# Kernel tuning notes

Hardware: AMD Instinct MI355X
Metric: run time of the kernel (lower is better)

Reference implementation:

```python
import jax, jax.numpy as jnp
import numpy as np

N = 200000          # nodes
E = 6400000         # edges (before self-loops)
L = 4               # layer_n
H = 9               # hidden_channels (hardcoded in module)
G = 2000            # graphs in batch
C = 2               # num_classes
NEG_SLOPE = 0.2     # GATConv default leaky_relu slope for attention logits


def setup_inputs() -> dict:
    key = jax.random.key(0)
    ks = jax.random.split(key, 9)
    x = jax.random.normal(ks[0], (N, H), dtype=jnp.float32)
    edge_index = jax.random.randint(ks[1], (2, E), 0, N, dtype=jnp.int32)
    batch = jnp.sort(jax.random.randint(ks[2], (N,), 0, G, dtype=jnp.int32))
    W = jax.random.normal(ks[3], (L, H, H), dtype=jnp.float32) * 0.3
    att_src = jax.random.normal(ks[4], (L, H), dtype=jnp.float32) * 0.3
    att_dst = jax.random.normal(ks[5], (L, H), dtype=jnp.float32) * 0.3
    bias = jax.random.normal(ks[6], (L, H), dtype=jnp.float32) * 0.1
    fc_w = jax.random.normal(ks[7], (L * H, C), dtype=jnp.float32) * 0.2
    fc_b = jax.random.normal(ks[8], (C,), dtype=jnp.float32) * 0.1
    return dict(x=x, edge_index=edge_index, batch=batch, W=W,
                att_src=att_src, att_dst=att_dst, bias=bias,
                fc_w=fc_w, fc_b=fc_b)


def _gat_layer(x, W_l, a_src, a_dst, b_l, src, dst, n):
    # h: [N, H] transformed features (linear, no bias per PyG default)
    h = x @ W_l
    alpha_s = h @ a_src            # [N]
    alpha_d = h @ a_dst            # [N]
    # attention logits per edge (src -> dst), GAT softmax grouped by dst
    e = jax.nn.leaky_relu(alpha_s[src] + alpha_d[dst], NEG_SLOPE)  # [E']
    e = e - jax.ops.segment_max(e, dst, num_segments=n)[dst]
    w = jnp.exp(e)
    denom = jax.ops.segment_sum(w, dst, num_segments=n)[dst]
    alpha = w / denom              # [E']
    out = jax.ops.segment_sum(alpha[:, None] * h[src], dst, num_segments=n)
    return out + b_l


def reference(x, edge_index, batch, W, att_src, att_dst, bias, fc_w, fc_b):
    n = x.shape[0]
    loops = jnp.arange(n, dtype=edge_index.dtype)
    src = jnp.concatenate([edge_index[0], loops])  # add_self_loops=True
    dst = jnp.concatenate([edge_index[1], loops])
    jk = []
    h = x
    for l in range(L):
        h = _gat_layer(h, W[l], att_src[l], att_dst[l], bias[l], src, dst, n)
        h = jax.nn.relu(h)
        jk.append(h)
    jk = jnp.concatenate(jk, axis=1)               # [N, L*H]
    pooled = jax.ops.segment_max(jk, batch, num_segments=G)
    pooled = jnp.where(jnp.isfinite(pooled), pooled, 0.0)  # guard empty graphs
    # dropout is identity at inference
    return pooled @ fc_w + fc_b
```

## Files before the change

### kernel.cpp

```cpp
#include <hip/hip_runtime.h>
#include <hip/hip_fp16.h>

#define Nn 200000
#define Ee 6400000
#define EP 6600000
#define Hh 9
#define Ll 4
#define Gg 2000
#define Cc 2
#define JK 36
#define NCB ((Nn + 1023) >> 10)
#define EPB 8192
#define NBLKA ((EP + EPB - 1) / EPB)
#define NB ((Nn + 255) / 256)
#define NPB 64
#define NAB (Nn / NPB)
#define CAP 4096

union H2F { __half2 h; float f; };


__global__ __launch_bounds__(256) void k_count(
    const int* __restrict__ dst, int* __restrict__ ctot)
{
    __shared__ int lh[NCB];
    int t = threadIdx.x;
    if (t < NCB) lh[t] = 0;
    __syncthreads();
    int base = blockIdx.x * EPB;
    for (int j = 0; j < EPB; j += 256) {
        int e = base + j + t;
        if (e < EP) {
            int d = (e < Ee) ? dst[e] : (e - Ee);
            atomicAdd(&lh[d >> 10], 1);
        }
    }
    __syncthreads();
    if (t < NCB && lh[t]) atomicAdd(&ctot[t], lh[t]);
}

__global__ __launch_bounds__(256) void k_scan(
    const int* __restrict__ ctot, int* __restrict__ cbase,
    int* __restrict__ ccur, int* __restrict__ row_ptr)
{
    __shared__ int s[256];
    int t = threadIdx.x;
    int v = (t < NCB) ? ctot[t] : 0;
    s[t] = v; __syncthreads();
    for (int off = 1; off < 256; off <<= 1) {
        int u = (t >= off) ? s[t - off] : 0;
        __syncthreads();
        s[t] += u;
        __syncthreads();
    }
    if (t < NCB) { cbase[t] = s[t] - v; ccur[t] = s[t] - v; }
    if (t == 0) { cbase[NCB] = EP; row_ptr[Nn] = EP; }
}

__global__ __launch_bounds__(256) void kA_scatter(
    const int* __restrict__ src, const int* __restrict__ dst,
    int* __restrict__ ccur, unsigned* __restrict__ bucketed)
{
    __shared__ int lh[NCB];
    __shared__ int cur[NCB];
    int t = threadIdx.x;
    if (t < NCB) lh[t] = 0;
    __syncthreads();
    int base = blockIdx.x * EPB;
    for (int j = 0; j < EPB; j += 256) {
        int e = base + j + t;
        if (e < EP) {
            int d = (e < Ee) ? dst[e] : (e - Ee);
            atomicAdd(&lh[d >> 10], 1);
        }
    }
    __syncthreads();
    if (t < NCB) cur[t] = atomicAdd(&ccur[t], lh[t]);
    __syncthreads();
    for (int j = 0; j < EPB; j += 256) {
        int e = base + j + t;
        if (e < EP) {
            int s, d;
            if (e < Ee) { s = src[e]; d = dst[e]; } else { s = e - Ee; d = s; }
            int pos = atomicAdd(&cur[d >> 10], 1);
            bucketed[pos] = (unsigned)s | ((unsigned)(d & 1023) << 18);
        }
    }
}

__global__ __launch_bounds__(1024) void kB_csr(
    const unsigned* __restrict__ bucketed, const int* __restrict__ cbase,
    int* __restrict__ row_ptr, int* __restrict__ csr_src)
{
    __shared__ int bh[1024];
    __shared__ int cur[1024];
    int k = blockIdx.x;
    int beg = cbase[k], end = cbase[k + 1];
    int t = threadIdx.x;
    bh[t] = 0;
    __syncthreads();
    for (int i = beg + t; i < end; i += 1024)
        atomicAdd(&bh[(bucketed[i] >> 18) & 1023], 1);
    __syncthreads();
    int v = bh[t];
    for (int off = 1; off < 1024; off <<= 1) {
        int u = (t >= off) ? bh[t - off] : 0;
        __syncthreads();
        bh[t] += u;
        __syncthreads();
    }
    int pos0 = beg + bh[t] - v;
    int node = (k << 10) + t;
    if (node < Nn) row_ptr[node] = pos0;
    cur[t] = pos0;
    __syncthreads();
    for (int i = beg + t; i < end; i += 1024) {
        unsigned p = bucketed[i];
        int pos = atomicAdd(&cur[(p >> 18) & 1023], 1);
        csr_src[pos] = (int)(p & 0x3FFFFu);
    }
}


__global__ __launch_bounds__(256) void k_transform(
    const float* __restrict__ xin, int xstride,
    const float* __restrict__ Wl,
    const float* __restrict__ asrc, const float* __restrict__ adst,
    float* __restrict__ h)
{
    int i = blockIdx.x * blockDim.x + threadIdx.x;
    if (i >= Nn) return;
    const float* xp = xin + (size_t)i * xstride;
    float xi[Hh];
#pragma unroll
    for (int k = 0; k < Hh; ++k) xi[k] = xp[k];
    float hv[Hh];
#pragma unroll
    for (int j = 0; j < Hh; ++j) {
        float s = 0.f;
#pragma unroll
        for (int k = 0; k < Hh; ++k) s += xi[k] * Wl[k * Hh + j];
        hv[j] = s;
    }
    float as = 0.f, ad = 0.f;
#pragma unroll
    for (int j = 0; j < Hh; ++j) { as += hv[j] * asrc[j]; ad += hv[j] * adst[j]; }
    H2F u01, u23, u45, u67, u8p;
    u01.h = __floats2half2_rn(hv[0], hv[1]);
    u23.h = __floats2half2_rn(hv[2], hv[3]);
    u45.h = __floats2half2_rn(hv[4], hv[5]);
    u67.h = __floats2half2_rn(hv[6], hv[7]);
    u8p.h = __floats2half2_rn(hv[8], 0.f);
    float4* hp = (float4*)(h + ((size_t)i << 3));
    hp[0] = make_float4(u01.f, u23.f, u45.f, u67.f);
    hp[1] = make_float4(u8p.f, as, ad, 0.f);
}

__global__ __launch_bounds__(256) void k_node_agg(
    const int* __restrict__ rp, const int* __restrict__ csr,
    const float* __restrict__ h, const float* __restrict__ biasl,
    float* __restrict__ jk, int l)
{
    __shared__ int scsr[CAP];
    __shared__ int srp[NPB + 1];
    const int nbase = blockIdx.x * NPB;
    const int t = threadIdx.x;
    if (t <= NPB) srp[t] = rp[nbase + t];
    __syncthreads();
    const int beg_blk = srp[0];
    const int nseg = srp[NPB] - beg_blk;
    const bool use_lds = (nseg <= CAP);
    if (use_lds)
        for (int j = t; j < nseg; j += 256) scsr[j] = csr[beg_blk + j];
    __syncthreads();

    const int ni = t >> 2;
    const int q  = t & 3;
    const int i  = nbase + ni;
    const float c = h[((size_t)i << 3) + 6];
    float a0=0,a1=0,a2=0,a3=0,a4=0,a5=0,a6=0,a7=0,a8=0,den=0;
    if (use_lds) {
        int idx = srp[ni] - beg_blk + q;
        const int iend = srp[ni + 1] - beg_blk;
        int s = (idx < iend) ? scsr[idx] : 0;
        while (idx < iend) {
            int nidx = idx + 4;
            int sn = (nidx < iend) ? scsr[nidx] : 0;
            const float4* hp = (const float4*)(h + ((size_t)s << 3));
            float4 F0 = hp[0], F1 = hp[1];
            float lg = F1.y + c;
            lg = lg > 0.f ? lg : 0.2f * lg;
            float w = __expf(lg);
            H2F u; float2 p;
            u.f = F0.x; p = __half22float2(u.h); a0 += w*p.x; a1 += w*p.y;
            u.f = F0.y; p = __half22float2(u.h); a2 += w*p.x; a3 += w*p.y;
            u.f = F0.z; p = __half22float2(u.h); a4 += w*p.x; a5 += w*p.y;
            u.f = F0.w; p = __half22float2(u.h); a6 += w*p.x; a7 += w*p.y;
            u.f = F1.x; p = __half22float2(u.h); a8 += w*p.x;
            den += w;
            idx = nidx; s = sn;
        }
    } else {
        for (int e = srp[ni] + q; e < srp[ni + 1]; e += 4) {
            int s = csr[e];
            const float4* hp = (const float4*)(h + ((size_t)s << 3));
            float4 F0 = hp[0], F1 = hp[1];
            float lg = F1.y + c;
            lg = lg > 0.f ? lg : 0.2f * lg;
            float w = __expf(lg);
            H2F u; float2 p;
            u.f = F0.x; p = __half22float2(u.h); a0 += w*p.x; a1 += w*p.y;
            u.f = F0.y; p = __half22float2(u.h); a2 += w*p.x; a3 += w*p.y;
            u.f = F0.z; p = __half22float2(u.h); a4 += w*p.x; a5 += w*p.y;
            u.f = F0.w; p = __half22float2(u.h); a6 += w*p.x; a7 += w*p.y;
            u.f = F1.x; p = __half22float2(u.h); a8 += w*p.x;
            den += w;
        }
    }
#pragma unroll
    for (int m = 1; m <= 2; m <<= 1) {
        a0 += __shfl_xor(a0, m); a1 += __shfl_xor(a1, m);
        a2 += __shfl_xor(a2, m); a3 += __shfl_xor(a3, m);
        a4 += __shfl_xor(a4, m); a5 += __shfl_xor(a5, m);
        a6 += __shfl_xor(a6, m); a7 += __shfl_xor(a7, m);
        a8 += __shfl_xor(a8, m); den += __shfl_xor(den, m);
    }
    if (q == 0) {
        float inv = 1.f / den;
        float* jp = jk + (size_t)i * JK + l * Hh;
        float o;
        o = a0*inv + biasl[0]; jp[0] = fmaxf(o, 0.f);
        o = a1*inv + biasl[1]; jp[1] = fmaxf(o, 0.f);
        o = a2*inv + biasl[2]; jp[2] = fmaxf(o, 0.f);
        o = a3*inv + biasl[3]; jp[3] = fmaxf(o, 0.f);
        o = a4*inv + biasl[4]; jp[4] = fmaxf(o, 0.f);
        o = a5*inv + biasl[5]; jp[5] = fmaxf(o, 0.f);
        o = a6*inv + biasl[6]; jp[6] = fmaxf(o, 0.f);
        o = a7*inv + biasl[7]; jp[7] = fmaxf(o, 0.f);
        o = a8*inv + biasl[8]; jp[8] = fmaxf(o, 0.f);
    }
}


__global__ __launch_bounds__(256) void k_graph_ptr(
    const int* __restrict__ batch, int* __restrict__ gp)
{
    int i = blockIdx.x * 256 + threadIdx.x;
    if (i >= Nn) return;
    int b = batch[i];
    if (i == 0) {
        for (int g = 0; g <= b; ++g) gp[g] = 0;
    } else {
        int pb = batch[i - 1];
        for (int g = pb + 1; g <= b; ++g) gp[g] = i;
    }
    if (i == Nn - 1) {
        for (int g = b + 1; g <= Gg; ++g) gp[g] = Nn;
    }
}

__global__ __launch_bounds__(256) void k_pool_seg(
    const float* __restrict__ jk, const int* __restrict__ gp,
    float* __restrict__ pooled)
{
    int t = blockIdx.x * 256 + threadIdx.x;
    if (t >= Gg * JK) return;
    int g = t / JK, col = t - g * JK;
    int beg = gp[g], end = gp[g + 1];
    float m = 0.f;
    for (int i = beg; i < end; ++i)
        m = fmaxf(m, jk[(size_t)i * JK + col]);
    pooled[t] = m;
}

__global__ __launch_bounds__(256) void k_fc(
    const float* __restrict__ pooled, const float* __restrict__ fcw,
    const float* __restrict__ fcb, float* __restrict__ out)
{
    int t = blockIdx.x * blockDim.x + threadIdx.x;
    if (t >= Gg * Cc) return;
    int g = t / Cc, c = t - g * Cc;
    float s = fcb[c];
    const float* pp = pooled + (size_t)g * JK;
#pragma unroll
    for (int j = 0; j < JK; ++j) s += pp[j] * fcw[j * Cc + c];
    out[t] = s;
}

extern "C" void kernel_launch(void* const* d_in, const int* in_sizes, int n_in,
                              void* d_out, int out_size, void* d_ws, size_t ws_size,
                              hipStream_t stream) {
    const float* x      = (const float*)d_in[0];
    const int*   ei     = (const int*)d_in[1];
    const int*   batch  = (const int*)d_in[2];
    const float* W      = (const float*)d_in[3];
    const float* a_src  = (const float*)d_in[4];
    const float* a_dst  = (const float*)d_in[5];
    const float* bias   = (const float*)d_in[6];
    const float* fc_w   = (const float*)d_in[7];
    const float* fc_b   = (const float*)d_in[8];
    float* out = (float*)d_out;

    float* ws        = (float*)d_ws;
    float* h         = ws;
    float* jk        = h + (size_t)Nn * 8;
    float* pooled    = jk + (size_t)Nn * JK;
    int* row_ptr     = (int*)(pooled + (size_t)Gg * JK);
    int* gp          = row_ptr + Nn + 1;
    int* ctot        = gp + Gg + 1;
    int* cbase       = ctot + NCB;
    int* ccur        = cbase + NCB + 1;
    int* csr_src     = ccur + NCB;
    unsigned* bucketed = (unsigned*)jk;

    const int* srcp = ei;
    const int* dstp = ei + Ee;

    hipMemsetAsync(ctot, 0, NCB * sizeof(int), stream);
    k_count   <<<NBLKA, 256, 0, stream>>>(dstp, ctot);
    k_scan    <<<1, 256, 0, stream>>>(ctot, cbase, ccur, row_ptr);
    kA_scatter<<<NBLKA, 256, 0, stream>>>(srcp, dstp, ccur, bucketed);
    kB_csr    <<<NCB, 1024, 0, stream>>>(bucketed, cbase, row_ptr, csr_src);

    for (int l = 0; l < Ll; ++l) {
        const float* xin = (l == 0) ? x : (jk + (size_t)(l - 1) * Hh);
        int xstride      = (l == 0) ? Hh : JK;
        k_transform<<<NB, 256, 0, stream>>>(xin, xstride, W + l * Hh * Hh,
                                            a_src + l * Hh, a_dst + l * Hh, h);
        k_node_agg<<<NAB, 256, 0, stream>>>(row_ptr, csr_src,
                                            h, bias + l * Hh, jk, l);
    }
    k_graph_ptr<<<NB, 256, 0, stream>>>(batch, gp);
    k_pool_seg<<<(Gg * JK + 255) / 256, 256, 0, stream>>>(jk, gp, pooled);
    k_fc<<<(Gg * Cc + 255) / 256, 256, 0, stream>>>(pooled, fc_w, fc_b, out);
}
```

Measured before the change: 586.5 us.

## Stage bucketed edges in LDS for coalesced writes; use 8 lanes per node

The scatter kernel now sorts each block's edges into an LDS buffer by coarse destination bucket, using a local prefix scan. It then writes them out contiguously per bucket through a binary-search offset lookup, replacing scattered global writes made through shared atomic cursors. The aggregation kernel halves nodes per block and assigns 8 lanes per node instead of 4, with the shuffle reduction widened to match. This trades a larger LDS footprint (32KB buffer) and extra binary-search work for better write coalescing and more parallelism per high-degree node.

```diff
diff --git a/kernel.cpp b/kernel.cpp
--- a/kernel.cpp
+++ b/kernel.cpp
@@ -13,9 +13,9 @@
 #define EPB 8192
 #define NBLKA ((EP + EPB - 1) / EPB)
 #define NB ((Nn + 255) / 256)
-#define NPB 64
+#define NPB 32
 #define NAB (Nn / NPB)
-#define CAP 4096
+#define CAP 3072
 
 union H2F { __half2 h; float f; };
 
@@ -61,30 +61,56 @@
     const int* __restrict__ src, const int* __restrict__ dst,
     int* __restrict__ ccur, unsigned* __restrict__ bucketed)
 {
+    __shared__ unsigned pbuf[EPB];
     __shared__ int lh[NCB];
-    __shared__ int cur[NCB];
+    __shared__ int lbase[NCB + 1];
+    __shared__ int delta[NCB];
     int t = threadIdx.x;
     if (t < NCB) lh[t] = 0;
     __syncthreads();
-    int base = blockIdx.x * EPB;
-    for (int j = 0; j < EPB; j += 256) {
-        int e = base + j + t;
-        if (e < EP) {
-            int d = (e < Ee) ? dst[e] : (e - Ee);
-            atomicAdd(&lh[d >> 10], 1);
-        }
-    }
-    __syncthreads();
-    if (t < NCB) cur[t] = atomicAdd(&ccur[t], lh[t]);
-    __syncthreads();
-    for (int j = 0; j < EPB; j += 256) {
-        int e = base + j + t;
-        if (e < EP) {
-            int s, d;
-            if (e < Ee) { s = src[e]; d = dst[e]; } else { s = e - Ee; d = s; }
-            int pos = atomicAdd(&cur[d >> 10], 1);
-            bucketed[pos] = (unsigned)s | ((unsigned)(d & 1023) << 18);
-        }
+    const int base = blockIdx.x * EPB;
+    const int nseg = min(EPB, EP - base);
+    for (int j = t; j < nseg; j += 256) {
+        int e = base + j;
+        int d = (e < Ee) ? dst[e] : (e - Ee);
+        atomicAdd(&lh[d >> 10], 1);
+    }
+    __syncthreads();
+    {
+        __shared__ int s[256];
+        int v = (t < NCB) ? lh[t] : 0;
+        s[t] = v; __syncthreads();
+        for (int off = 1; off < 256; off <<= 1) {
+            int u = (t >= off) ? s[t - off] : 0;
+            __syncthreads();
+            s[t] += u;
+            __syncthreads();
+        }
+        if (t < NCB) {
+            int ex = s[t] - v;
+            lbase[t] = ex;
+            lh[t] = ex;
+            int g = v ? atomicAdd(&ccur[t], v) : 0;
+            delta[t] = g - ex;
+        }
+        if (t == 0) lbase[NCB] = nseg;
+    }
+    __syncthreads();
+    for (int j = t; j < nseg; j += 256) {
+        int e = base + j;
+        int s, d;
+        if (e < Ee) { s = src[e]; d = dst[e]; } else { s = e - Ee; d = s; }
+        int pos = atomicAdd(&lh[d >> 10], 1);
+        pbuf[pos] = (unsigned)s | ((unsigned)(d & 1023) << 18);
+    }
+    __syncthreads();
+    for (int j = t; j < nseg; j += 256) {
+        int lo = 0, hi = NCB - 1;
+        while (lo < hi) {
+            int mid = (lo + hi + 1) >> 1;
+            if (lbase[mid] <= j) lo = mid; else hi = mid - 1;
+        }
+        bucketed[delta[lo] + j] = pbuf[j];
     }
 }
 
@@ -174,8 +200,8 @@
         for (int j = t; j < nseg; j += 256) scsr[j] = csr[beg_blk + j];
     __syncthreads();
 
-    const int ni = t >> 2;
-    const int q  = t & 3;
+    const int ni = t >> 3;
+    const int q  = t & 7;
     const int i  = nbase + ni;
     const float c = h[((size_t)i << 3) + 6];
     float a0=0,a1=0,a2=0,a3=0,a4=0,a5=0,a6=0,a7=0,a8=0,den=0;
@@ -184,7 +210,7 @@
         const int iend = srp[ni + 1] - beg_blk;
         int s = (idx < iend) ? scsr[idx] : 0;
         while (idx < iend) {
-            int nidx = idx + 4;
+            int nidx = idx + 8;
             int sn = (nidx < iend) ? scsr[nidx] : 0;
             const float4* hp = (const float4*)(h + ((size_t)s << 3));
             float4 F0 = hp[0], F1 = hp[1];
@@ -201,7 +227,7 @@
             idx = nidx; s = sn;
         }
     } else {
-        for (int e = srp[ni] + q; e < srp[ni + 1]; e += 4) {
+        for (int e = srp[ni] + q; e < srp[ni + 1]; e += 8) {
             int s = csr[e];
             const float4* hp = (const float4*)(h + ((size_t)s << 3));
             float4 F0 = hp[0], F1 = hp[1];
@@ -218,7 +244,7 @@
         }
     }
 #pragma unroll
-    for (int m = 1; m <= 2; m <<= 1) {
+    for (int m = 1; m <= 4; m <<= 1) {
         a0 += __shfl_xor(a0, m); a1 += __shfl_xor(a1, m);
         a2 += __shfl_xor(a2, m); a3 += __shfl_xor(a3, m);
         a4 += __shfl_xor(a4, m); a5 += __shfl_xor(a5, m);
```

Result: faster. 554.1 us (-5.5%).
